# Optimization experiments

Measured on AMD Instinct MI355X. Metric: run time of the kernel, lower is better.

The kernel has to match this reference:

```python
import jax, jax.numpy as jnp
import numpy as np
import math

B, L, C, Hh, Ww = 1, 16, 32, 64, 64
Wf = Ww // 2 + 1
R = 16
GROUPS = 4
MID = 4  # max(C//16, 4)
DT_REF = 1.0
INJ_K = 2.0
EPS = 1e-5


def _conv2d(x, w, b):
    y = jax.lax.conv_general_dilated(x, w, (1, 1), 'SAME',
                                     dimension_numbers=('NCHW', 'OIHW', 'NCHW'))
    return y + b[None, :, None, None]


def _adaptive_avg_w(x, out_w):
    # adaptive avg pool along last axis (torch AdaptiveAvgPool semantics)
    w_in = x.shape[-1]
    cs = jnp.concatenate([jnp.zeros(x.shape[:-1] + (1,), x.dtype), jnp.cumsum(x, -1)], -1)
    starts = np.floor(np.arange(out_w) * w_in / out_w).astype(np.int32)
    ends = np.ceil((np.arange(out_w) + 1) * w_in / out_w).astype(np.int32)
    num = cs[..., ends] - cs[..., starts]
    den = jnp.asarray(ends - starts, x.dtype)
    return num / den


def setup_inputs() -> dict:
    key = jax.random.key(0)
    ks = jax.random.split(key, 24)
    s = 0.05
    inp = {}
    inp['x'] = jax.random.normal(ks[0], (B, C, L, Hh, Ww), jnp.float32)
    inp['dt'] = jax.random.uniform(ks[1], (B, L), jnp.float32, 0.1, 1.0)
    inp['conv1_w'] = jax.random.normal(ks[2], (C, C, 3, 3), jnp.float32) * s
    inp['conv1_b'] = jnp.zeros((C,), jnp.float32)
    inp['conv2_w'] = jax.random.normal(ks[3], (C, C, 3, 3), jnp.float32) * s
    inp['conv2_b'] = jnp.zeros((C,), jnp.float32)
    inp['gfc_w'] = jax.random.normal(ks[4], (C, C), jnp.float32) * s
    inp['gfc_b'] = jnp.zeros((C,), jnp.float32)
    inp['head_w'] = jax.random.normal(ks[5], (C * R * 3, C), jnp.float32) * 0.02
    hb = np.zeros((C, R, 3), np.float32); hb[..., 0] = 1.0; hb[..., 2] = -5.0
    inp['head_b'] = jnp.asarray(hb.reshape(-1))
    inp['mix_w'] = jnp.eye(2 * R, dtype=jnp.float32) + jax.random.normal(ks[6], (2 * R, 2 * R), jnp.float32) * 0.02
    inp['mix_b'] = jnp.zeros((2 * R,), jnp.float32)
    inp['rank_scale'] = jnp.ones((R,), jnp.float32)
    inp['proj_w'] = jax.random.normal(ks[7], (1, R), jnp.float32) * s
    inp['proj_b'] = jnp.zeros((1,), jnp.float32)
    inp['pif_w'] = jax.random.normal(ks[8], (C, C), jnp.float32) * s  # 1x1x1 Conv3d
    inp['pif_b'] = jnp.zeros((C,), jnp.float32)
    inp['gn_w'] = jnp.ones((C,), jnp.float32)
    inp['gn_b'] = jnp.zeros((C,), jnp.float32)
    inp['g1_w'] = jax.random.normal(ks[9], (MID, C), jnp.float32) * s
    inp['g1_b'] = jnp.zeros((MID,), jnp.float32)
    inp['g2_w'] = jax.random.normal(ks[10], (C, MID), jnp.float32) * s
    inp['g2_b'] = jnp.zeros((C,), jnp.float32)
    return inp


def _forward(x, dt, conv1_w, conv1_b, conv2_w, conv2_b, gfc_w, gfc_b, head_w, head_b,
             mix_w, mix_b, rank_scale, proj_w, proj_b, pif_w, pif_b, gn_w, gn_b,
             g1_w, g1_b, g2_w, g2_b):
    Bx, Cx, Lx, H, W = x.shape
    x_seq = jnp.transpose(x, (0, 2, 1, 3, 4))  # [B,L,C,H,W]
    # ---- DynamicsParameterEstimator on flattened [B*L,C,H,W] ----
    xf = x_seq.reshape(Bx * Lx, Cx, H, W)
    f = jax.nn.silu(_conv2d(xf, conv1_w, conv1_b))
    f = jax.nn.silu(_conv2d(f, conv2_w, conv2_b))
    glob = jax.nn.sigmoid(f.mean((2, 3)) @ gfc_w.T + gfc_b)  # [BL,C]
    f = f * glob[:, :, None, None]
    f = _adaptive_avg_w(f.mean(2), Wf)         # [BL,C,Wf]
    feat = jnp.transpose(f, (0, 2, 1))          # [BL,Wf,C]
    p = (feat @ head_w.T + head_b).reshape(Bx * Lx, Wf, Cx, R, 3)
    nu = jax.nn.softplus(p[..., 0]).reshape(Bx, Lx, Wf, Cx, R)
    th = (jnp.tanh(p[..., 1]) * math.pi).reshape(Bx, Lx, Wf, Cx, R)
    sg = jax.nn.sigmoid(p[..., 2]).reshape(Bx, Lx, Wf, Cx, R)
    nu = jnp.transpose(nu, (0, 1, 3, 2, 4))[:, :, :, None]  # [B,L,C,1,Wf,R]
    th = jnp.transpose(th, (0, 1, 3, 2, 4))[:, :, :, None]
    sg = jnp.transpose(sg, (0, 1, 3, 2, 4))[:, :, :, None]
    # ---- Koopman A (triton kernel math): exp(-nu*dt) * exp(i*theta*dt) ----
    dtb = dt[:, :, None, None, None, None]
    decay = jnp.exp(-nu * dtb)
    ang = th * dtb
    A = jax.lax.complex(decay * jnp.cos(ang), decay * jnp.sin(ang))  # [B,L,C,1,Wf,R]
    # ---- injection in rfft space, gated by dt ----
    g = 1.0 - jnp.exp(-INJ_K * jnp.clip(dt / max(DT_REF, 1e-6), 0.0))  # [B,L]
    xfreq = jnp.fft.rfft(x_seq, axis=-1)        # [B,L,C,H,Wf] complex
    u = sg * xfreq[..., None] * g[:, :, None, None, None, None]  # [B,L,C,H,Wf,R]
    # ---- parallel linear recurrence h_t = A_t h_{t-1} + u_t ----
    def combine(a, b):
        Aa, ua = a
        Ab, ub = b
        return (Ab * Aa, Ab * ua + ub)
    _, h = jax.lax.associative_scan(combine, (A, u), axis=1)  # h: [B,L,C,H,Wf,R]
    # ---- SpectralMixer over rank (real/imag stacked) ----
    hs = jnp.concatenate([h.real, h.imag], -1) @ mix_w.T + mix_b
    hr, hi = jnp.split(hs, 2, -1)
    h = jax.lax.complex(hr, hi) * rank_scale
    # ---- rank projection + irfft ----
    y = jnp.einsum('blchfr,r->blchf', h, proj_w[0].astype(h.dtype)) + proj_b[0]
    y = jnp.fft.irfft(y, n=W, axis=-1)          # [B,L,C,H,W]
    y = jnp.transpose(y, (0, 2, 1, 3, 4))        # [B,C,L,H,W]
    # ---- post_ifft_proj: 1x1x1 Conv3d ----
    y = jnp.einsum('bclhw,oc->bolhw', y, pif_w) + pif_b[None, :, None, None, None]
    # ---- SpatialGroupNorm (per-frame GroupNorm, 4 groups) ----
    z = jnp.transpose(y, (0, 2, 1, 3, 4)).reshape(Bx * Lx, GROUPS, (Cx // GROUPS) * H * W)
    mu = z.mean(-1, keepdims=True)
    var = z.var(-1, keepdims=True)
    z = (z - mu) / jnp.sqrt(var + EPS)
    z = z.reshape(Bx, Lx, Cx, H, W) * gn_w[None, None, :, None, None] + gn_b[None, None, :, None, None]
    y = jnp.transpose(z, (0, 2, 1, 3, 4))        # [B,C,L,H,W]
    # ---- LatitudeGating (squeeze-excite over W) ----
    ym = y.mean(-1)                              # [B,C,L,H]
    yg = jnp.transpose(ym, (0, 2, 3, 1))          # [B,L,H,C]
    yg = jax.nn.sigmoid(jax.nn.silu(yg @ g1_w.T + g1_b) @ g2_w.T + g2_b)
    gate = jnp.transpose(yg, (0, 3, 1, 2))[..., None]  # [B,C,L,H,1]
    return x + y * gate


def reference(x, dt, conv1_w, conv1_b, conv2_w, conv2_b, gfc_w, gfc_b, head_w, head_b,
              mix_w, mix_b, rank_scale, proj_w, proj_b, pif_w, pif_b, gn_w, gn_b,
              g1_w, g1_b, g2_w, g2_b):
    return _forward(x, dt, conv1_w, conv1_b, conv2_w, conv2_b, gfc_w, gfc_b, head_w,
                    head_b, mix_w, mix_b, rank_scale, proj_w, proj_b, pif_w, pif_b,
                    gn_w, gn_b, g1_w, g1_b, g2_w, g2_b)
```

## Files before the change

### kernel.cpp

```cpp
#include <hip/hip_runtime.h>
#include <hip/hip_bf16.h>
#include <math.h>

#define CC 32
#define LL 16
#define HH 64
#define WW 64
#define WF 33
#define RR 16
#define PI_F 3.14159265358979323846f

typedef __attribute__((ext_vector_type(8))) short short8;
typedef __attribute__((ext_vector_type(4))) float f32x4;

#define OFF_F1      0
#define OFF_COLSUM  2097152
#define OFF_FEAT    2130944
#define OFF_ARE     2147840
#define OFF_AIM     2418176
#define OFF_SGG     2688512
#define OFF_XFR     2958848
#define OFF_XFI     4040192
#define OFF_YFR     5121536
#define OFF_YFI     6202880
#define OFF_PART    2958848
#define OFF_Y1      2958848
#define OFF_Y2      0
#define OFF_GNM     7284224
#define OFF_GNR     7284288
#define OFF_YM      7284352
#define OFF_GATE    7317120
#define OFF_WVEC    7349888
#define OFF_WT      7350016

__device__ __forceinline__ float sigmoidf_(float x){ return 1.0f/(1.0f+expf(-x)); }
__device__ __forceinline__ unsigned short f2bf(float v){
    __hip_bfloat16 b = __float2bfloat16(v);
    return *reinterpret_cast<unsigned short*>(&b);
}
__device__ __forceinline__ float bf2f(unsigned short u){
    __hip_bfloat16 b = *reinterpret_cast<__hip_bfloat16*>(&u);
    return __bfloat162float(b);
}

__global__ void k_prep0(const float* __restrict__ mix_w, const float* __restrict__ mix_b,
                        const float* __restrict__ rank_scale, const float* __restrict__ proj_w,
                        const float* __restrict__ proj_b,
                        const float* __restrict__ c1w, const float* __restrict__ c2w,
                        float* __restrict__ ws){
    unsigned short* wt = (unsigned short*)(ws + OFF_WT);
    if (blockIdx.x == 0){
        float* wv = ws + OFF_WVEC;
        int t = threadIdx.x;
        if (t < 32){
            float sre=0.f, sim=0.f;
            for (int r=0;r<RR;r++){
                float a = proj_w[r]*rank_scale[r];
                sre += a*mix_w[r*2*RR + t];
                sim += a*mix_w[(RR+r)*2*RR + t];
            }
            wv[t] = sre; wv[32+t] = sim;
        }
        if (t == 0){
            float cre=0.f, cim=0.f;
            for (int r=0;r<RR;r++){
                float a = proj_w[r]*rank_scale[r];
                cre += a*mix_b[r];
                cim += a*mix_b[RR+r];
            }
            wv[64] = cre + proj_b[0]; wv[65] = cim;
        }
        return;
    }
    int i = (blockIdx.x-1)*256 + threadIdx.x;
    if (i < 18432){
        int which = (i >= 9216);
        int j = which ? i - 9216 : i;
        int je   = j & 7;
        int lane = (j >> 3) & 63;
        int ct   = (j >> 9) & 1;
        int tap  = j >> 10;
        int kh = tap/3, kw = tap - kh*3;
        int co = ct*16 + (lane & 15);
        int ci = (lane >> 4)*8 + je;
        const float* cw = which ? c2w : c1w;
        wt[i] = f2bf(cw[((co*CC + ci)*3 + kh)*3 + kw]);
        return;
    }
    i -= 18432;
    if (i < 10240){
        int j = i & 7, lane = (i>>3)&63, cch = (i>>9)&3, t = i>>11;
        int frow = t*16 + (lane & 15);
        int k = ((lane>>4)&3)*8 + j;
        int w = (cch & 1)*32 + k;
        float coef = 0.f;
        if (frow < 33)       coef =  cosf(2.0f*PI_F*(float)(frow*w)/64.0f);
        else if (frow < 66)  coef = -sinf(2.0f*PI_F*(float)((frow-33)*w)/64.0f);
        unsigned short hi = f2bf(coef);
        wt[18432 + i] = (cch < 2) ? hi : f2bf(coef - bf2f(hi));
        return;
    }
    i -= 10240;
    if (i < 12288){
        int wtile = i / 3072;
        int rem = i - wtile*3072;
        int ch = rem >> 9;
        int ll = rem & 511;
        int lane = ll >> 3, j = ll & 7;
        int w = wtile*16 + (lane & 15);
        int k = (ch % 3)*32 + ((lane>>4)&3)*8 + j;
        float coef = 0.f;
        if (k < 33){
            float s = (k==0 || k==32) ? 1.f : 2.f;
            coef = s*cosf(2.0f*PI_F*(float)(k*w)/64.0f)*(1.0f/64.0f);
        } else if (k < 66){
            int f = k - 33;
            float s = (f==0 || f==32) ? 1.f : 2.f;
            coef = -s*sinf(2.0f*PI_F*(float)(f*w)/64.0f)*(1.0f/64.0f);
        }
        unsigned short hi = f2bf(coef);
        wt[18432 + 10240 + i] = (ch < 3) ? hi : f2bf(coef - bf2f(hi));
        return;
    }
}

__global__ __launch_bounds__(256, 4) void k_conv1m(const float* __restrict__ x,
                                                   const unsigned short* __restrict__ wt,
                                                   const float* __restrict__ cb,
                                                   unsigned short* __restrict__ f1p){
    __shared__ __align__(16) unsigned short xs[3*66*32];
    __shared__ __align__(16) unsigned short pw[9216];

    const int tid  = threadIdx.x;
    const int l    = blockIdx.x >> 6;
    const int h    = blockIdx.x & 63;
    const int wid  = tid >> 6;
    const int lane = tid & 63;
    const int col  = lane & 15;
    const int kgrp = lane >> 4;

    {
        const unsigned int* src = (const unsigned int*)wt;
        unsigned int* dst = (unsigned int*)pw;
        #pragma unroll
        for (int j = 0; j < 18; ++j) dst[tid + j*256] = src[tid + j*256];
    }
    {
        const int rr = tid >> 6;
        const int w  = tid & 63;
        if (rr < 3){
            int hh = h - 1 + rr;
            bool hv = (hh >= 0 && hh < HH);
            const float* sp = x + (long)l*HH*WW + hh*WW + w;
            int wIdx = 1 + w;
            #pragma unroll
            for (int cib = 0; cib < 4; ++cib){
                float v[8];
                #pragma unroll
                for (int k = 0; k < 8; ++k)
                    v[k] = hv ? sp[(long)(cib*8 + k)*LL*HH*WW] : 0.f;
                uint4 p;
                p.x = (unsigned)f2bf(v[0]) | ((unsigned)f2bf(v[1])<<16);
                p.y = (unsigned)f2bf(v[2]) | ((unsigned)f2bf(v[3])<<16);
                p.z = (unsigned)f2bf(v[4]) | ((unsigned)f2bf(v[5])<<16);
                p.w = (unsigned)f2bf(v[6]) | ((unsigned)f2bf(v[7])<<16);
                int cs = cib ^ (wIdx & 3);
                *(uint4*)&xs[(rr*66 + wIdx)*32 + cs*8] = p;
            }
        } else {
            int s = tid & 63;
            if (s < 24){
                int row = s >> 3, rest = s & 7;
                int wIdx = (rest >> 2) ? 65 : 0;
                int cib = rest & 3;
                *(uint4*)&xs[(row*66 + wIdx)*32 + cib*8] = make_uint4(0,0,0,0);
            }
        }
    }
    __syncthreads();

    #pragma unroll
    for (int u = 0; u < 2; ++u){
        int unit = wid + u*4;
        int ct   = unit >> 2;
        int wt16 = unit & 3;
        int colw = wt16*16 + col;
        f32x4 acc = {0.f,0.f,0.f,0.f};
        #pragma unroll
        for (int kh = 0; kh < 3; ++kh){
            #pragma unroll
            for (int kw = 0; kw < 3; ++kw){
                int wIdx = colw + kw;
                int cs = kgrp ^ (wIdx & 3);
                short8 b = *(const short8*)&xs[(kh*66 + wIdx)*32 + cs*8];
                short8 a = *(const short8*)&pw[((kh*3+kw)*2 + ct)*512 + lane*8];
                acc = __builtin_amdgcn_mfma_f32_16x16x32_bf16(a, b, acc, 0, 0, 0);
            }
        }
        int co0 = ct*16 + kgrp*4;
        float o[4];
        #pragma unroll
        for (int r = 0; r < 4; ++r){
            float v = acc[r] + cb[co0+r];
            o[r] = v * sigmoidf_(v);
        }
        uint2 pk;
        pk.x = (unsigned)f2bf(o[0]) | ((unsigned)f2bf(o[1])<<16);
        pk.y = (unsigned)f2bf(o[2]) | ((unsigned)f2bf(o[3])<<16);
        *(uint2*)&f1p[(((long)l*HH + h)*WW + colw)*32 + co0] = pk;
    }
}

__global__ __launch_bounds__(256, 4) void k_conv2m(const unsigned short* __restrict__ f1p,
                                                   const unsigned short* __restrict__ wt,
                                                   const float* __restrict__ cb,
                                                   float* __restrict__ ws){
    __shared__ __align__(16) unsigned short xs[3*66*32];
    __shared__ __align__(16) unsigned short pw[9216];
    __shared__ float red[CC*WW];

    const int tid  = threadIdx.x;
    const int l    = blockIdx.x >> 6;
    const int h    = blockIdx.x & 63;
    const int wid  = tid >> 6;
    const int lane = tid & 63;
    const int col  = lane & 15;
    const int kgrp = lane >> 4;

    {
        const unsigned int* src = (const unsigned int*)wt;
        unsigned int* dst = (unsigned int*)pw;
        #pragma unroll
        for (int j = 0; j < 18; ++j) dst[tid + j*256] = src[tid + j*256];
    }
    {
        const int rr = tid >> 6;
        const int w  = tid & 63;
        if (rr < 3){
            int hh = h - 1 + rr;
            bool hv = (hh >= 0 && hh < HH);
            const uint4* sp = (const uint4*)&f1p[(((long)l*HH + hh)*WW + w)*32];
            int wIdx = 1 + w;
            #pragma unroll
            for (int cib = 0; cib < 4; ++cib){
                uint4 p = hv ? sp[cib] : make_uint4(0,0,0,0);
                int cs = cib ^ (wIdx & 3);
                *(uint4*)&xs[(rr*66 + wIdx)*32 + cs*8] = p;
            }
        } else {
            int s = tid & 63;
            if (s < 24){
                int row = s >> 3, rest = s & 7;
                int wIdx = (rest >> 2) ? 65 : 0;
                int cib = rest & 3;
                *(uint4*)&xs[(row*66 + wIdx)*32 + cib*8] = make_uint4(0,0,0,0);
            }
        }
    }
    __syncthreads();

    #pragma unroll
    for (int u = 0; u < 2; ++u){
        int unit = wid + u*4;
        int ct   = unit >> 2;
        int wt16 = unit & 3;
        int colw = wt16*16 + col;
        f32x4 acc = {0.f,0.f,0.f,0.f};
        #pragma unroll
        for (int kh = 0; kh < 3; ++kh){
            #pragma unroll
            for (int kw = 0; kw < 3; ++kw){
                int wIdx = colw + kw;
                int cs = kgrp ^ (wIdx & 3);
                short8 b = *(const short8*)&xs[(kh*66 + wIdx)*32 + cs*8];
                short8 a = *(const short8*)&pw[((kh*3+kw)*2 + ct)*512 + lane*8];
                acc = __builtin_amdgcn_mfma_f32_16x16x32_bf16(a, b, acc, 0, 0, 0);
            }
        }
        int co0 = ct*16 + kgrp*4;
        #pragma unroll
        for (int r = 0; r < 4; ++r){
            float v = acc[r] + cb[co0+r];
            red[(co0+r)*WW + colw] = v * sigmoidf_(v);
        }
    }
    __syncthreads();
    float4* p4 = (float4*)(ws + OFF_PART + ((long)(l*HH + h))*2048);
    const float4* r4 = (const float4*)red;
    p4[tid]       = r4[tid];
    p4[tid + 256] = r4[tid + 256];
}

__global__ void k_colred(float* __restrict__ ws){
    int b = blockIdx.x;
    int l = b >> 5, c = b & 31;
    int w = threadIdx.x;
    const float* p = ws + OFF_PART + (long)l*HH*2048 + c*WW + w;
    float s = 0.f;
    #pragma unroll 8
    for (int h = 0; h < HH; ++h) s += p[h*2048];
    ws[OFF_COLSUM + (l*CC + c)*WW + w] = s;
}

__global__ void k_globfeat(const float* __restrict__ gfc_w, const float* __restrict__ gfc_b,
                           float* __restrict__ ws){
    __shared__ float gs[CC], gl[CC];
    int l = blockIdx.x;
    int tid = threadIdx.x;
    if (tid < 32){
        const float* cs = ws + OFF_COLSUM + (l*CC+tid)*WW;
        float s = 0.f;
        for (int w=0;w<WW;w++) s += cs[w];
        gs[tid] = s;
    }
    __syncthreads();
    if (tid < 32){
        float acc = gfc_b[tid];
        for (int i=0;i<CC;i++) acc += gs[i]*(1.0f/4096.0f)*gfc_w[tid*CC+i];
        gl[tid] = sigmoidf_(acc);
    }
    __syncthreads();
    for (int i = tid; i < WF*CC; i += 256){
        int c = i & 31, wf = i >> 5;
        int s = (wf*64)/33;
        int e = ((wf+1)*64 + 32)/33;
        const float* cs = ws + OFF_COLSUM + (l*CC+c)*WW;
        float sum = 0.f;
        for (int w=s;w<e;w++) sum += cs[w];
        ws[OFF_FEAT + (l*WF+wf)*CC + c] = gl[c] * sum / (64.0f*(float)(e-s));
    }
}

__global__ void k_head(const float* __restrict__ hw, const float* __restrict__ hb,
                       const float* __restrict__ dt, float* __restrict__ ws){
    int t = blockIdx.x*blockDim.x + threadIdx.x;
    if (t >= LL*WF*CC*RR) return;
    int r = t & 15, c = (t>>4) & 31;
    int lw_ = t >> 9;
    int wf = lw_ % WF, l = lw_ / WF;
    const float* feat = ws + OFF_FEAT + (l*WF+wf)*CC;
    int j0 = (c*RR + r)*3;
    const float* w0 = hw + j0*CC;
    float p0=hb[j0], p1=hb[j0+1], p2=hb[j0+2];
    for (int i=0;i<CC;i++){
        float fv = feat[i];
        p0 += fv*w0[i]; p1 += fv*w0[CC+i]; p2 += fv*w0[2*CC+i];
    }
    float nu = fmaxf(p0,0.f) + log1pf(expf(-fabsf(p0)));
    float th = tanhf(p1)*PI_F;
    float sg = sigmoidf_(p2);
    float dtv = dt[l];
    float decay = expf(-nu*dtv);
    float ang = th*dtv;
    float g = 1.0f - expf(-2.0f*fmaxf(dtv,0.f));
    int idx = ((l*CC+c)*WF+wf)*RR + r;
    ws[OFF_ARE+idx] = decay*cosf(ang);
    ws[OFF_AIM+idx] = decay*sinf(ang);
    ws[OFF_SGG+idx] = sg*g;
}

__global__ __launch_bounds__(256, 4) void k_rfftm(const float* __restrict__ x,
                                                  const unsigned short* __restrict__ at,
                                                  float* __restrict__ ws){
    __shared__ __align__(16) unsigned short xs[HH*68];
    int b = blockIdx.x; int l = b >> 5, c = b & 31;
    int tid = threadIdx.x;
    const int wid  = tid >> 6;
    const int lane = tid & 63;
    const int col  = lane & 15;
    const int kgrp = lane >> 4;

    const float* xp = x + (long)(c*LL + l)*HH*WW;
    for (int i = tid; i < HH*WW; i += 256){
        int h = i >> 6, w = i & 63;
        xs[h*68 + w] = f2bf(xp[i]);
    }
    __syncthreads();

    float* xfr = ws + OFF_XFR + (long)(l*CC + c)*HH*WF;
    float* xfi = ws + OFF_XFI + (long)(l*CC + c)*HH*WF;
    #pragma unroll
    for (int q = 0; q < 5; ++q){
        int unit = wid + q*4;
        int ftile = unit >> 2;
        int htile = unit & 3;
        f32x4 acc = {0.f,0.f,0.f,0.f};
        #pragma unroll
        for (int cch = 0; cch < 4; ++cch){
            short8 a = *(const short8*)&at[(((ftile*4 + cch)*64) + lane)*8];
            short8 bb = *(const short8*)&xs[(htile*16 + col)*68 + (cch & 1)*32 + kgrp*8];
            acc = __builtin_amdgcn_mfma_f32_16x16x32_bf16(a, bb, acc, 0, 0, 0);
        }
        int h = htile*16 + col;
        #pragma unroll
        for (int r = 0; r < 4; ++r){
            int fr = ftile*16 + kgrp*4 + r;
            if (fr < 33)      xfr[fr*HH + h] = acc[r];
            else if (fr < 66) xfi[(fr-33)*HH + h] = acc[r];
        }
    }
}

__global__ __launch_bounds__(256) void k_scan(float* __restrict__ ws){
    __shared__ float lA[LL*RR], lI[LL*RR], lS[LL*RR];
    __shared__ float wv[66];
    int b = blockIdx.x;
    int c = b / WF, f = b - c*WF;
    int tid = threadIdx.x;
    if (tid < 66) wv[tid] = ws[OFF_WVEC + tid];
    {
        int l = tid >> 4, r = tid & 15;
        int src = ((l*CC + c)*WF + f)*RR + r;
        lA[tid] = ws[OFF_ARE + src];
        lI[tid] = ws[OFF_AIM + src];
        lS[tid] = ws[OFF_SGG + src];
    }
    __syncthreads();
    const int h  = tid >> 2;
    const int rq = tid & 3;
    float sre[4] = {0,0,0,0}, sim[4] = {0,0,0,0};
    float w0_[4], w1_[4], w2_[4], w3_[4];
    #pragma unroll
    for (int q=0;q<4;q++){
        int r = rq*4 + q;
        w0_[q]=wv[r]; w1_[q]=wv[16+r]; w2_[q]=wv[32+r]; w3_[q]=wv[48+r];
    }
    const float cre = wv[64], cim = wv[65];
    const long fh = (long)(c*WF + f)*HH + h;
    #pragma unroll 1
    for (int l=0;l<LL;l++){
        float xr = ws[OFF_XFR + l*(CC*HH*WF) + fh];
        float xi = ws[OFF_XFI + l*(CC*HH*WF) + fh];
        float yr = 0.f, yi = 0.f;
        #pragma unroll
        for (int q=0;q<4;q++){
            int r = rq*4 + q;
            float a = lA[l*16+r], ii = lI[l*16+r], s = lS[l*16+r];
            float nre = a*sre[q] - ii*sim[q] + s*xr;
            float nim = a*sim[q] + ii*sre[q] + s*xi;
            sre[q]=nre; sim[q]=nim;
            yr += w0_[q]*nre + w1_[q]*nim;
            yi += w2_[q]*nre + w3_[q]*nim;
        }
        yr += __shfl_xor(yr, 1); yr += __shfl_xor(yr, 2);
        yi += __shfl_xor(yi, 1); yi += __shfl_xor(yi, 2);
        if (rq == 0){
            ws[OFF_YFR + l*(CC*HH*WF) + fh] = yr + cre;
            ws[OFF_YFI + l*(CC*HH*WF) + fh] = yi + cim;
        }
    }
}

__global__ __launch_bounds__(256, 4) void k_irfftm(const unsigned short* __restrict__ btb,
                                                   float* __restrict__ ws){
    __shared__ __align__(16) unsigned short mh[HH*100];
    int b = blockIdx.x; int l = b >> 5, c = b & 31;
    int tid = threadIdx.x;
    const int wid  = tid >> 6;
    const int lane = tid & 63;
    const int col  = lane & 15;
    const int kgrp = lane >> 4;

    const float* Yr = ws + OFF_YFR + (long)(l*CC + c)*HH*WF;
    const float* Yi = ws + OFF_YFI + (long)(l*CC + c)*HH*WF;
    for (int i = tid; i < 33*64; i += 256){
        int f = i >> 6, h = i & 63;
        mh[h*100 + f]      = f2bf(Yr[i]);
        mh[h*100 + 33 + f] = f2bf(Yi[i]);
    }
    for (int i = tid; i < 64*34; i += 256){
        int h = i / 34, f = 66 + (i - (i/34)*34);
        mh[h*100 + f] = 0;
    }
    __syncthreads();

    float* y1 = ws + OFF_Y1 + (long)(l*CC + c)*HH*WW;
    #pragma unroll
    for (int q = 0; q < 4; ++q){
        int unit = wid + q*4;
        int htile = unit >> 2;
        int wtile = unit & 3;
        f32x4 acc = {0.f,0.f,0.f,0.f};
        #pragma unroll
        for (int ch = 0; ch < 6; ++ch){
            int kof = (ch % 3)*32 + kgrp*8;
            short8 a = *(const short8*)&mh[(htile*16 + col)*100 + kof];
            short8 bb = *(const short8*)&btb[(((wtile*6 + ch)*64) + lane)*8];
            acc = __builtin_amdgcn_mfma_f32_16x16x32_bf16(a, bb, acc, 0, 0, 0);
        }
        int w = wtile*16 + col;
        #pragma unroll
        for (int r = 0; r < 4; ++r){
            int h = htile*16 + kgrp*4 + r;
            y1[h*WW + w] = acc[r];
        }
    }
}

__global__ void k_pif(const float* __restrict__ pw, const float* __restrict__ pb,
                      float* __restrict__ ws){
    __shared__ float row[CC][WW];
    int b = blockIdx.x; int l = b>>6, h = b&63;
    int tid = threadIdx.x;
    for (int k=0;k<8;k++){
        int i = tid + k*256;
        int ci = i>>6, w = i&63;
        row[ci][w] = ws[OFF_Y1 + ((l*CC+ci)*HH + h)*WW + w];
    }
    __syncthreads();
    for (int k=0;k<8;k++){
        int i = tid + k*256;
        int o = i>>6, w = i&63;
        float acc = pb[o];
        #pragma unroll
        for (int ci=0;ci<CC;ci++) acc += pw[o*CC+ci]*row[ci][w];
        ws[OFF_Y2 + ((l*CC+o)*HH + h)*WW + w] = acc;
        float s = acc;
        s += __shfl_down(s, 32, 64); s += __shfl_down(s, 16, 64);
        s += __shfl_down(s, 8, 64);  s += __shfl_down(s, 4, 64);
        s += __shfl_down(s, 2, 64);  s += __shfl_down(s, 1, 64);
        if ((tid & 63) == 0) ws[OFF_YM + (l*HH+h)*CC + o] = s*(1.0f/64.0f);
    }
}

__global__ void k_gnstat(float* __restrict__ ws){
    __shared__ float rs[256], rq[256];
    int b = blockIdx.x; int l = b>>2, g = b&3;
    const float* z = ws + OFF_Y2 + (l*CC + g*8)*HH*WW;
    int tid = threadIdx.x;
    float s=0.f, q=0.f;
    for (int i=tid;i<8*HH*WW;i+=256){ float v=z[i]; s+=v; q+=v*v; }
    rs[tid]=s; rq[tid]=q; __syncthreads();
    for (int off=128; off>0; off>>=1){
        if (tid<off){ rs[tid]+=rs[tid+off]; rq[tid]+=rq[tid+off]; }
        __syncthreads();
    }
    if (tid==0){
        float mean = rs[0]/32768.0f;
        float var = rq[0]/32768.0f - mean*mean;
        ws[OFF_GNM + b] = mean;
        ws[OFF_GNR + b] = rsqrtf(var + 1e-5f);
    }
}

__global__ void k_gate(const float* __restrict__ g1w, const float* __restrict__ g1b,
                       const float* __restrict__ g2w, const float* __restrict__ g2b,
                       const float* __restrict__ gnw, const float* __restrict__ gnb,
                       float* __restrict__ ws){
    int t = blockIdx.x*256 + threadIdx.x;
    if (t >= LL*HH*CC) return;
    int c = t & 31, h = (t>>5)&63, l = t>>11;
    const float* ym = ws + OFF_YM + (l*HH+h)*CC;
    float mus[4], rsd[4];
    #pragma unroll
    for (int g=0; g<4; ++g){ mus[g] = ws[OFF_GNM + l*4+g]; rsd[g] = ws[OFF_GNR + l*4+g]; }
    float ymn[CC];
    #pragma unroll
    for (int i=0;i<CC;i++){
        int g = i>>3;
        ymn[i] = (ym[i] - mus[g])*rsd[g]*gnw[i] + gnb[i];
    }
    float mid[4];
    #pragma unroll
    for (int m=0;m<4;m++){
        float a = g1b[m];
        #pragma unroll
        for (int i=0;i<CC;i++) a += ymn[i]*g1w[m*CC+i];
        mid[m] = a*sigmoidf_(a);
    }
    float a = g2b[c];
    #pragma unroll
    for (int m=0;m<4;m++) a += mid[m]*g2w[c*4+m];
    ws[OFF_GATE + t] = sigmoidf_(a);
}

__global__ void k_final(const float* __restrict__ x, float* __restrict__ out,
                        const float* __restrict__ gnw, const float* __restrict__ gnb,
                        const float* __restrict__ ws){
    int t = blockIdx.x*256 + threadIdx.x;
    int n = t*4;
    int h = (n>>6)&63, l = (n>>12)&15, c = n>>16;
    int g = c>>3;
    float mu = ws[OFF_GNM + l*4+g], rstd = ws[OFF_GNR + l*4+g];
    float gw = gnw[c]*rstd, gb = gnb[c] - mu*gnw[c]*rstd;
    float4 z  = *(const float4*)(ws + OFF_Y2 + (((l*CC+c)*HH+h)*WW) + (n&63));
    float  gt = ws[OFF_GATE + (l*HH+h)*CC + c];
    float4 xv = *(const float4*)(x + n);
    float4 o;
    o.x = xv.x + (z.x*gw+gb)*gt; o.y = xv.y + (z.y*gw+gb)*gt;
    o.z = xv.z + (z.z*gw+gb)*gt; o.w = xv.w + (z.w*gw+gb)*gt;
    *(float4*)(out + n) = o;
}

extern "C" void kernel_launch(void* const* d_in, const int* in_sizes, int n_in,
                              void* d_out, int out_size, void* d_ws, size_t ws_size,
                              hipStream_t stream){
    const float* x    = (const float*)d_in[0];
    const float* dt   = (const float*)d_in[1];
    const float* c1w  = (const float*)d_in[2];
    const float* c1b  = (const float*)d_in[3];
    const float* c2w  = (const float*)d_in[4];
    const float* c2b  = (const float*)d_in[5];
    const float* gfcw = (const float*)d_in[6];
    const float* gfcb = (const float*)d_in[7];
    const float* hw   = (const float*)d_in[8];
    const float* hb   = (const float*)d_in[9];
    const float* mixw = (const float*)d_in[10];
    const float* mixb = (const float*)d_in[11];
    const float* rs   = (const float*)d_in[12];
    const float* pjw  = (const float*)d_in[13];
    const float* pjb  = (const float*)d_in[14];
    const float* pifw = (const float*)d_in[15];
    const float* pifb = (const float*)d_in[16];
    const float* gnw  = (const float*)d_in[17];
    const float* gnb  = (const float*)d_in[18];
    const float* g1w  = (const float*)d_in[19];
    const float* g1b  = (const float*)d_in[20];
    const float* g2w  = (const float*)d_in[21];
    const float* g2b  = (const float*)d_in[22];
    float* ws  = (float*)d_ws;
    float* out = (float*)d_out;
    unsigned short* wt  = (unsigned short*)(ws + OFF_WT);
    unsigned short* at  = wt + 18432;
    unsigned short* btb = wt + 18432 + 10240;
    unsigned short* f1p = (unsigned short*)(ws + OFF_F1);

    k_prep0   <<<161,  256, 0, stream>>>(mixw, mixb, rs, pjw, pjb, c1w, c2w, ws);
    k_conv1m  <<<1024, 256, 0, stream>>>(x, wt, c1b, f1p);
    k_conv2m  <<<1024, 256, 0, stream>>>(f1p, wt + 9216, c2b, ws);
    k_colred  <<<512,  64,  0, stream>>>(ws);
    k_globfeat<<<16,   256, 0, stream>>>(gfcw, gfcb, ws);
    k_head    <<<1056, 256, 0, stream>>>(hw, hb, dt, ws);
    k_rfftm   <<<512,  256, 0, stream>>>(x, at, ws);
    k_scan    <<<1056, 256, 0, stream>>>(ws);
    k_irfftm  <<<512,  256, 0, stream>>>(btb, ws);
    k_pif     <<<1024, 256, 0, stream>>>(pifw, pifb, ws);
    k_gnstat  <<<64,   256, 0, stream>>>(ws);
    k_gate    <<<128,  256, 0, stream>>>(g1w, g1b, g2w, g2b, gnw, gnb, ws);
    k_final   <<<2048, 256, 0, stream>>>(x, out, gnw, gnb, ws);
}
```

Baseline: 239.0 us.

## Process two output rows per conv block and fuse GroupNorm stats into pif

Result: faster. 208.2 us (-12.9%).

```diff
diff --git a/kernel.cpp b/kernel.cpp
--- a/kernel.cpp
+++ b/kernel.cpp
@@ -32,6 +32,7 @@
 #define OFF_GATE    7317120
 #define OFF_WVEC    7349888
 #define OFF_WT      7350016
+#define OFF_YQ      7370496
 
 __device__ __forceinline__ float sigmoidf_(float x){ return 1.0f/(1.0f+expf(-x)); }
 __device__ __forceinline__ unsigned short f2bf(float v){
@@ -128,12 +129,12 @@
                                                    const unsigned short* __restrict__ wt,
                                                    const float* __restrict__ cb,
                                                    unsigned short* __restrict__ f1p){
-    __shared__ __align__(16) unsigned short xs[3*66*32];
+    __shared__ __align__(16) unsigned short xs[4*66*32];
     __shared__ __align__(16) unsigned short pw[9216];
 
     const int tid  = threadIdx.x;
-    const int l    = blockIdx.x >> 6;
-    const int h    = blockIdx.x & 63;
+    const int l    = blockIdx.x >> 5;
+    const int h0   = (blockIdx.x & 31)*2;
     const int wid  = tid >> 6;
     const int lane = tid & 63;
     const int col  = lane & 15;
@@ -148,42 +149,40 @@
     {
         const int rr = tid >> 6;
         const int w  = tid & 63;
-        if (rr < 3){
-            int hh = h - 1 + rr;
-            bool hv = (hh >= 0 && hh < HH);
-            const float* sp = x + (long)l*HH*WW + hh*WW + w;
-            int wIdx = 1 + w;
+        int hh = h0 - 1 + rr;
+        bool hv = (hh >= 0 && hh < HH);
+        const float* sp = x + (long)l*HH*WW + hh*WW + w;
+        int wIdx = 1 + w;
+        #pragma unroll
+        for (int cib = 0; cib < 4; ++cib){
+            float v[8];
             #pragma unroll
-            for (int cib = 0; cib < 4; ++cib){
-                float v[8];
-                #pragma unroll
-                for (int k = 0; k < 8; ++k)
-                    v[k] = hv ? sp[(long)(cib*8 + k)*LL*HH*WW] : 0.f;
-                uint4 p;
-                p.x = (unsigned)f2bf(v[0]) | ((unsigned)f2bf(v[1])<<16);
-                p.y = (unsigned)f2bf(v[2]) | ((unsigned)f2bf(v[3])<<16);
-                p.z = (unsigned)f2bf(v[4]) | ((unsigned)f2bf(v[5])<<16);
-                p.w = (unsigned)f2bf(v[6]) | ((unsigned)f2bf(v[7])<<16);
-                int cs = cib ^ (wIdx & 3);
-                *(uint4*)&xs[(rr*66 + wIdx)*32 + cs*8] = p;
-            }
-        } else {
-            int s = tid & 63;
-            if (s < 24){
-                int row = s >> 3, rest = s & 7;
-                int wIdx = (rest >> 2) ? 65 : 0;
-                int cib = rest & 3;
-                *(uint4*)&xs[(row*66 + wIdx)*32 + cib*8] = make_uint4(0,0,0,0);
-            }
-        }
-    }
-    __syncthreads();
-
-    #pragma unroll
-    for (int u = 0; u < 2; ++u){
+            for (int k = 0; k < 8; ++k)
+                v[k] = hv ? sp[(long)(cib*8 + k)*LL*HH*WW] : 0.f;
+            uint4 p;
+            p.x = (unsigned)f2bf(v[0]) | ((unsigned)f2bf(v[1])<<16);
+            p.y = (unsigned)f2bf(v[2]) | ((unsigned)f2bf(v[3])<<16);
+            p.z = (unsigned)f2bf(v[4]) | ((unsigned)f2bf(v[5])<<16);
+            p.w = (unsigned)f2bf(v[6]) | ((unsigned)f2bf(v[7])<<16);
+            int cs = cib ^ (wIdx & 3);
+            *(uint4*)&xs[(rr*66 + wIdx)*32 + cs*8] = p;
+        }
+    }
+    if (tid < 32){
+        int row = tid >> 3, rest = tid & 7;
+        int wIdx = (rest >> 2) ? 65 : 0;
+        int cib = rest & 3;
+        *(uint4*)&xs[(row*66 + wIdx)*32 + cib*8] = make_uint4(0,0,0,0);
+    }
+    __syncthreads();
+
+    #pragma unroll
+    for (int u = 0; u < 4; ++u){
         int unit = wid + u*4;
-        int ct   = unit >> 2;
-        int wt16 = unit & 3;
+        int hloc = unit >> 3;
+        int rem  = unit & 7;
+        int ct   = rem >> 2;
+        int wt16 = rem & 3;
         int colw = wt16*16 + col;
         f32x4 acc = {0.f,0.f,0.f,0.f};
         #pragma unroll
@@ -192,12 +191,13 @@
             for (int kw = 0; kw < 3; ++kw){
                 int wIdx = colw + kw;
                 int cs = kgrp ^ (wIdx & 3);
-                short8 b = *(const short8*)&xs[(kh*66 + wIdx)*32 + cs*8];
+                short8 b = *(const short8*)&xs[((hloc+kh)*66 + wIdx)*32 + cs*8];
                 short8 a = *(const short8*)&pw[((kh*3+kw)*2 + ct)*512 + lane*8];
                 acc = __builtin_amdgcn_mfma_f32_16x16x32_bf16(a, b, acc, 0, 0, 0);
             }
         }
         int co0 = ct*16 + kgrp*4;
+        int h = h0 + hloc;
         float o[4];
         #pragma unroll
         for (int r = 0; r < 4; ++r){
@@ -215,13 +215,12 @@
                                                    const unsigned short* __restrict__ wt,
                                                    const float* __restrict__ cb,
                                                    float* __restrict__ ws){
-    __shared__ __align__(16) unsigned short xs[3*66*32];
+    __shared__ __align__(16) unsigned short xs[4*66*32];
     __shared__ __align__(16) unsigned short pw[9216];
-    __shared__ float red[CC*WW];
 
     const int tid  = threadIdx.x;
-    const int l    = blockIdx.x >> 6;
-    const int h    = blockIdx.x & 63;
+    const int l    = blockIdx.x >> 5;
+    const int h0   = (blockIdx.x & 31)*2;
     const int wid  = tid >> 6;
     const int lane = tid & 63;
     const int col  = lane & 15;
@@ -236,34 +235,32 @@
     {
         const int rr = tid >> 6;
         const int w  = tid & 63;
-        if (rr < 3){
-            int hh = h - 1 + rr;
-            bool hv = (hh >= 0 && hh < HH);
-            const uint4* sp = (const uint4*)&f1p[(((long)l*HH + hh)*WW + w)*32];
-            int wIdx = 1 + w;
-            #pragma unroll
-            for (int cib = 0; cib < 4; ++cib){
-                uint4 p = hv ? sp[cib] : make_uint4(0,0,0,0);
-                int cs = cib ^ (wIdx & 3);
-                *(uint4*)&xs[(rr*66 + wIdx)*32 + cs*8] = p;
-            }
-        } else {
-            int s = tid & 63;
-            if (s < 24){
-                int row = s >> 3, rest = s & 7;
-                int wIdx = (rest >> 2) ? 65 : 0;
-                int cib = rest & 3;
-                *(uint4*)&xs[(row*66 + wIdx)*32 + cib*8] = make_uint4(0,0,0,0);
-            }
-        }
-    }
-    __syncthreads();
-
-    #pragma unroll
-    for (int u = 0; u < 2; ++u){
+        int hh = h0 - 1 + rr;
+        bool hv = (hh >= 0 && hh < HH);
+        const uint4* sp = (const uint4*)&f1p[(((long)l*HH + hh)*WW + w)*32];
+        int wIdx = 1 + w;
+        #pragma unroll
+        for (int cib = 0; cib < 4; ++cib){
+            uint4 p = hv ? sp[cib] : make_uint4(0,0,0,0);
+            int cs = cib ^ (wIdx & 3);
+            *(uint4*)&xs[(rr*66 + wIdx)*32 + cs*8] = p;
+        }
+    }
+    if (tid < 32){
+        int row = tid >> 3, rest = tid & 7;
+        int wIdx = (rest >> 2) ? 65 : 0;
+        int cib = rest & 3;
+        *(uint4*)&xs[(row*66 + wIdx)*32 + cib*8] = make_uint4(0,0,0,0);
+    }
+    __syncthreads();
+
+    #pragma unroll
+    for (int u = 0; u < 4; ++u){
         int unit = wid + u*4;
-        int ct   = unit >> 2;
-        int wt16 = unit & 3;
+        int hloc = unit >> 3;
+        int rem  = unit & 7;
+        int ct   = rem >> 2;
+        int wt16 = rem & 3;
         int colw = wt16*16 + col;
         f32x4 acc = {0.f,0.f,0.f,0.f};
         #pragma unroll
@@ -272,23 +269,20 @@
             for (int kw = 0; kw < 3; ++kw){
                 int wIdx = colw + kw;
                 int cs = kgrp ^ (wIdx & 3);
-                short8 b = *(const short8*)&xs[(kh*66 + wIdx)*32 + cs*8];
+                short8 b = *(const short8*)&xs[((hloc+kh)*66 + wIdx)*32 + cs*8];
                 short8 a = *(const short8*)&pw[((kh*3+kw)*2 + ct)*512 + lane*8];
                 acc = __builtin_amdgcn_mfma_f32_16x16x32_bf16(a, b, acc, 0, 0, 0);
             }
         }
         int co0 = ct*16 + kgrp*4;
+        int h = h0 + hloc;
+        float* pp = ws + OFF_PART + ((long)(l*HH + h))*2048 + colw;
         #pragma unroll
         for (int r = 0; r < 4; ++r){
             float v = acc[r] + cb[co0+r];
-            red[(co0+r)*WW + colw] = v * sigmoidf_(v);
-        }
-    }
-    __syncthreads();
-    float4* p4 = (float4*)(ws + OFF_PART + ((long)(l*HH + h))*2048);
-    const float4* r4 = (const float4*)red;
-    p4[tid]       = r4[tid];
-    p4[tid + 256] = r4[tid + 256];
+            pp[(co0+r)*WW] = v * sigmoidf_(v);
+        }
+    }
 }
 
 __global__ void k_colred(float* __restrict__ ws){
@@ -515,29 +509,40 @@
         #pragma unroll
         for (int ci=0;ci<CC;ci++) acc += pw[o*CC+ci]*row[ci][w];
         ws[OFF_Y2 + ((l*CC+o)*HH + h)*WW + w] = acc;
-        float s = acc;
-        s += __shfl_down(s, 32, 64); s += __shfl_down(s, 16, 64);
-        s += __shfl_down(s, 8, 64);  s += __shfl_down(s, 4, 64);
-        s += __shfl_down(s, 2, 64);  s += __shfl_down(s, 1, 64);
-        if ((tid & 63) == 0) ws[OFF_YM + (l*HH+h)*CC + o] = s*(1.0f/64.0f);
-    }
-}
-
-__global__ void k_gnstat(float* __restrict__ ws){
+        float s = acc, q = acc*acc;
+        s += __shfl_down(s, 32, 64); q += __shfl_down(q, 32, 64);
+        s += __shfl_down(s, 16, 64); q += __shfl_down(q, 16, 64);
+        s += __shfl_down(s,  8, 64); q += __shfl_down(q,  8, 64);
+        s += __shfl_down(s,  4, 64); q += __shfl_down(q,  4, 64);
+        s += __shfl_down(s,  2, 64); q += __shfl_down(q,  2, 64);
+        s += __shfl_down(s,  1, 64); q += __shfl_down(q,  1, 64);
+        if ((tid & 63) == 0){
+            ws[OFF_YM + (l*HH+h)*CC + o] = s*(1.0f/64.0f);
+            ws[OFF_YQ + (l*HH+h)*CC + o] = q;
+        }
+    }
+}
+
+__global__ void k_gnred(float* __restrict__ ws){
     __shared__ float rs[256], rq[256];
     int b = blockIdx.x; int l = b>>2, g = b&3;
-    const float* z = ws + OFF_Y2 + (l*CC + g*8)*HH*WW;
     int tid = threadIdx.x;
     float s=0.f, q=0.f;
-    for (int i=tid;i<8*HH*WW;i+=256){ float v=z[i]; s+=v; q+=v*v; }
+    for (int j = tid; j < 512; j += 256){
+        int h = j >> 3, cc = j & 7;
+        int off = (l*HH+h)*CC + g*8 + cc;
+        s += ws[OFF_YM + off];
+        q += ws[OFF_YQ + off];
+    }
     rs[tid]=s; rq[tid]=q; __syncthreads();
     for (int off=128; off>0; off>>=1){
         if (tid<off){ rs[tid]+=rs[tid+off]; rq[tid]+=rq[tid+off]; }
         __syncthreads();
     }
     if (tid==0){
-        float mean = rs[0]/32768.0f;
-        float var = rq[0]/32768.0f - mean*mean;
+        float mean = rs[0]*(1.0f/512.0f);
+        float ex2  = rq[0]*(1.0f/32768.0f);
+        float var = ex2 - mean*mean;
         ws[OFF_GNM + b] = mean;
         ws[OFF_GNR + b] = rsqrtf(var + 1e-5f);
     }
@@ -626,8 +631,8 @@
     unsigned short* f1p = (unsigned short*)(ws + OFF_F1);
 
     k_prep0   <<<161,  256, 0, stream>>>(mixw, mixb, rs, pjw, pjb, c1w, c2w, ws);
-    k_conv1m  <<<1024, 256, 0, stream>>>(x, wt, c1b, f1p);
-    k_conv2m  <<<1024, 256, 0, stream>>>(f1p, wt + 9216, c2b, ws);
+    k_conv1m  <<<512,  256, 0, stream>>>(x, wt, c1b, f1p);
+    k_conv2m  <<<512,  256, 0, stream>>>(f1p, wt + 9216, c2b, ws);
     k_colred  <<<512,  64,  0, stream>>>(ws);
     k_globfeat<<<16,   256, 0, stream>>>(gfcw, gfcb, ws);
     k_head    <<<1056, 256, 0, stream>>>(hw, hb, dt, ws);
@@ -635,7 +640,7 @@
     k_scan    <<<1056, 256, 0, stream>>>(ws);
     k_irfftm  <<<512,  256, 0, stream>>>(btb, ws);
     k_pif     <<<1024, 256, 0, stream>>>(pifw, pifb, ws);
-    k_gnstat  <<<64,   256, 0, stream>>>(ws);
+    k_gnred   <<<64,   256, 0, stream>>>(ws);
     k_gate    <<<128,  256, 0, stream>>>(g1w, g1b, g2w, g2b, gnw, gnb, ws);
     k_final   <<<2048, 256, 0, stream>>>(x, out, gnw, gnb, ws);
 }
```
